# Performance work log

Measured on AMD Instinct MI355X. Metric: run time of the kernel, lower is better.

Reference implementation:

```python
import jax, jax.numpy as jnp
import numpy as np

B, T, IN, H = 131072, 8, 6, 64

def _lstm_layer(x, Wih, Whh, bih, bhh):
    # x: (B, T, in) -> h_seq: (B, T, H). PyTorch gate order: i, f, g, o.
    xg = jnp.einsum('bti,gi->btg', x, Wih) + bih + bhh  # (B, T, 4H)
    Bsz = x.shape[0]
    h0 = jnp.zeros((Bsz, Whh.shape[1]), x.dtype)
    c0 = jnp.zeros_like(h0)
    def step(carry, xg_t):
        h, c = carry
        g = xg_t + h @ Whh.T  # (B, 4H)
        i, f, gg, o = jnp.split(g, 4, axis=-1)
        i = jax.nn.sigmoid(i); f = jax.nn.sigmoid(f)
        gg = jnp.tanh(gg); o = jax.nn.sigmoid(o)
        c = f * c + i * gg
        h = o * jnp.tanh(c)
        return (h, c), h
    _, h_seq = jax.lax.scan(step, (h0, c0), jnp.swapaxes(xg, 0, 1))  # (T, B, H)
    return jnp.swapaxes(h_seq, 0, 1)

def setup_inputs() -> dict:
    key = jax.random.key(0)
    ks = jax.random.split(key, 11)
    s_in = 1.0 / np.sqrt(H)
    u = lambda k, shape: jax.random.uniform(k, shape, jnp.float32, -s_in, s_in)
    return {
        'x': jax.random.normal(ks[0], (B, T, IN), jnp.float32),
        'Wih0': u(ks[1], (4 * H, IN)), 'Whh0': u(ks[2], (4 * H, H)),
        'bih0': u(ks[3], (4 * H,)),   'bhh0': u(ks[4], (4 * H,)),
        'Wih1': u(ks[5], (4 * H, H)), 'Whh1': u(ks[6], (4 * H, H)),
        'bih1': u(ks[7], (4 * H,)),   'bhh1': u(ks[8], (4 * H,)),
        'Wfc': u(ks[9], (1, H)),      'bfc': u(ks[10], (1,)),
    }

def reference(x, Wih0, Whh0, bih0, bhh0, Wih1, Whh1, bih1, bhh1, Wfc, bfc):
    h1 = _lstm_layer(x, Wih0, Whh0, bih0, bhh0)   # (B, T, H)
    # inter-layer dropout & output dropout are identity in eval mode
    h2 = _lstm_layer(h1, Wih1, Whh1, bih1, bhh1)  # (B, T, H)
    last = h2[:, -1, :]                            # (B, H)
    out = last @ Wfc.T + bfc                       # (B, 1)
    return out[:, 0]
```

## Files before the change

### kernel.cpp

```cpp
#include <hip/hip_runtime.h>

#define BLOCK 256
#define TT 8
#define INP 6
#define HDIM 64
#define LDH 72

typedef _Float16 f16;
typedef __attribute__((ext_vector_type(8))) _Float16 f16x8;
typedef __attribute__((ext_vector_type(16))) float f32x16;

#define WIH0_OFF 0
#define WHH0_OFF 4096
#define WIH1_OFF 20480
#define WHH1_OFF 36864
#define H0_OFF   53248
#define H1_OFF   (53248 + 128*LDH)
#define NF16     (53248 + 2*128*LDH)
#define NF32     640

__device__ __forceinline__ float sigm(float x){
    return __builtin_amdgcn_rcpf(1.0f + __builtin_exp2f(-1.442695040888963f*x));
}
__device__ __forceinline__ float ftanh(float x){
    return 1.0f - 2.0f*__builtin_amdgcn_rcpf(1.0f + __builtin_exp2f(2.885390081777927f*x));
}

__global__ void __launch_bounds__(BLOCK, 1)
lstm_mfma(const float* __restrict__ x,
          const float* __restrict__ Wih0, const float* __restrict__ Whh0,
          const float* __restrict__ bih0, const float* __restrict__ bhh0,
          const float* __restrict__ Wih1, const float* __restrict__ Whh1,
          const float* __restrict__ bih1, const float* __restrict__ bhh1,
          const float* __restrict__ Wfc,  const float* __restrict__ bfc,
          float* __restrict__ out)
{
    extern __shared__ char smem[];
    float* fbias = (float*)smem;
    float* fwfc  = fbias + 512;
    f16*   fh    = (f16*)(smem + NF32*4);

    const int tid = threadIdx.x;

    for (int i = tid; i < 3*16384; i += BLOCK){
        int m  = i >> 14;
        int j  = i & 16383;
        int e  = j & 7;
        int l2 = (j >> 3) & 63;
        int fg = j >> 9;
        int n  = (fg >> 2)*32 + (l2 & 31);
        int k  = (fg & 3)*16 + (l2 >> 5)*8 + e;
        const float* W = (m==0)? Whh0 : (m==1)? Wih1 : Whh1;
        int off = (m==0)? WHH0_OFF : (m==1)? WIH1_OFF : WHH1_OFF;
        fh[off + fg*512 + (j & 511)] = (f16)W[n*HDIM + k];
    }
    for (int i = tid; i < 4096; i += BLOCK){
        int e = i & 7, l2 = (i >> 3) & 63, nt = i >> 9;
        int n = nt*32 + (l2 & 31);
        int k = (l2 >> 5)*8 + e;
        fh[WIH0_OFF + nt*512 + (i & 511)] = (k < INP)? (f16)Wih0[n*INP + k] : (f16)0.0f;
    }
    for (int i = tid; i < 256; i += BLOCK){
        fbias[i]       = bih0[i] + bhh0[i];
        fbias[256 + i] = bih1[i] + bhh1[i];
    }
    if (tid < 64) fwfc[tid] = Wfc[tid];
    if (tid == 0) fwfc[64] = bfc[0];
    __syncthreads();

    const int l     = tid & 63;
    const int w     = tid >> 6;
    const int rlo   = l & 31;
    const int khalf = l >> 5;
    const int row0  = blockIdx.x*128 + w*32;

    f16* h0p = fh + H0_OFF + (w*32)*LDH;
    f16* h1p = fh + H1_OFF + (w*32)*LDH;

    float c0[32], c1[32];
#pragma unroll
    for (int i=0;i<32;i++){ c0[i]=0.f; c1[i]=0.f; }

    const float* xrow = x + (size_t)(row0 + rlo)*TT*INP;

#pragma unroll 1
    for (int t=0;t<TT;t++){
        f16x8 xf;
#pragma unroll
        for (int i2=0;i2<8;i2++) xf[i2] = (f16)0.f;
        if (khalf == 0){
            const float* xp = xrow + t*INP;
            xf[0]=(f16)xp[0]; xf[1]=(f16)xp[1]; xf[2]=(f16)xp[2];
            xf[3]=(f16)xp[3]; xf[4]=(f16)xp[4]; xf[5]=(f16)xp[5];
        }

        f32x16 acc[8];
#pragma unroll
        for (int nt=0;nt<8;nt++){
            float bv = fbias[nt*32 + rlo];
#pragma unroll
            for (int r=0;r<16;r++) acc[nt][r] = bv;
        }
#pragma unroll
        for (int nt=0;nt<8;nt++){
            f16x8 bf = *(const f16x8*)(fh + WIH0_OFF + nt*512 + l*8);
            acc[nt] = __builtin_amdgcn_mfma_f32_32x32x16_f16(xf, bf, acc[nt], 0,0,0);
        }
        if (t > 0){
#pragma unroll
            for (int kt=0;kt<4;kt++){
                f16x8 hf = *(const f16x8*)(h0p + rlo*LDH + kt*16 + khalf*8);
#pragma unroll
                for (int nt=0;nt<8;nt++){
                    f16x8 bf = *(const f16x8*)(fh + WHH0_OFF + (nt*4+kt)*512 + l*8);
                    acc[nt] = __builtin_amdgcn_mfma_f32_32x32x16_f16(hf, bf, acc[nt], 0,0,0);
                }
            }
        }
#pragma unroll
        for (int s=0;s<2;s++){
#pragma unroll
            for (int r=0;r<16;r++){
                float ig = sigm (acc[0+s][r]);
                float fg = sigm (acc[2+s][r]);
                float gg = ftanh(acc[4+s][r]);
                float og = sigm (acc[6+s][r]);
                float c  = fg*c0[s*16+r] + ig*gg;
                c0[s*16+r] = c;
                float hv = og*ftanh(c);
                h0p[((r&3) + 8*(r>>2) + 4*khalf)*LDH + rlo + 32*s] = (f16)hv;
            }
        }
        __syncthreads();

#pragma unroll
        for (int nt=0;nt<8;nt++){
            float bv = fbias[256 + nt*32 + rlo];
#pragma unroll
            for (int r=0;r<16;r++) acc[nt][r] = bv;
        }
#pragma unroll
        for (int kt=0;kt<4;kt++){
            f16x8 hf = *(const f16x8*)(h0p + rlo*LDH + kt*16 + khalf*8);
#pragma unroll
            for (int nt=0;nt<8;nt++){
                f16x8 bf = *(const f16x8*)(fh + WIH1_OFF + (nt*4+kt)*512 + l*8);
                acc[nt] = __builtin_amdgcn_mfma_f32_32x32x16_f16(hf, bf, acc[nt], 0,0,0);
            }
        }
        if (t > 0){
#pragma unroll
            for (int kt=0;kt<4;kt++){
                f16x8 hf = *(const f16x8*)(h1p + rlo*LDH + kt*16 + khalf*8);
#pragma unroll
                for (int nt=0;nt<8;nt++){
                    f16x8 bf = *(const f16x8*)(fh + WHH1_OFF + (nt*4+kt)*512 + l*8);
                    acc[nt] = __builtin_amdgcn_mfma_f32_32x32x16_f16(hf, bf, acc[nt], 0,0,0);
                }
            }
        }
#pragma unroll
        for (int s=0;s<2;s++){
#pragma unroll
            for (int r=0;r<16;r++){
                float ig = sigm (acc[0+s][r]);
                float fg = sigm (acc[2+s][r]);
                float gg = ftanh(acc[4+s][r]);
                float og = sigm (acc[6+s][r]);
                float c  = fg*c1[s*16+r] + ig*gg;
                c1[s*16+r] = c;
                float hv = og*ftanh(c);
                h1p[((r&3) + 8*(r>>2) + 4*khalf)*LDH + rlo + 32*s] = (f16)hv;
            }
        }
        __syncthreads();
    }

    if (tid < 128){
        const f16* hp = fh + H1_OFF + tid*LDH;
        float sacc = fwfc[64];
#pragma unroll
        for (int u=0;u<HDIM;u++) sacc += fwfc[u]*(float)hp[u];
        out[(size_t)blockIdx.x*128 + tid] = sacc;
    }
}

extern "C" void kernel_launch(void* const* d_in, const int* in_sizes, int n_in,
                              void* d_out, int out_size, void* d_ws, size_t ws_size,
                              hipStream_t stream) {
    const float* x    = (const float*)d_in[0];
    const float* Wih0 = (const float*)d_in[1];
    const float* Whh0 = (const float*)d_in[2];
    const float* bih0 = (const float*)d_in[3];
    const float* bhh0 = (const float*)d_in[4];
    const float* Wih1 = (const float*)d_in[5];
    const float* Whh1 = (const float*)d_in[6];
    const float* bih1 = (const float*)d_in[7];
    const float* bhh1 = (const float*)d_in[8];
    const float* Wfc  = (const float*)d_in[9];
    const float* bfc  = (const float*)d_in[10];
    float* out = (float*)d_out;

    const int B = in_sizes[0] / (TT*INP);
    const size_t shmem = (size_t)NF32*4 + (size_t)NF16*2;
    hipFuncSetAttribute(reinterpret_cast<const void*>(lstm_mfma),
                        hipFuncAttributeMaxDynamicSharedMemorySize, (int)shmem);
    lstm_mfma<<<dim3(B/128), dim3(BLOCK), shmem, stream>>>(
        x, Wih0, Whh0, bih0, bhh0, Wih1, Whh1, bih1, bhh1, Wfc, bfc, out);
}
```

Measured before the change: 482.5 us.

## Swap MFMA operands so hidden state stays in registers, drop LDS h buffers

The MFMA operand roles are swapped: weights become the A operand and the hidden state the B operand, so each gate output lands in the layout the next step needs. The hidden state is then repacked in registers with a cross-half shuffle instead of going through LDS, which removes both __syncthreads per step. Biases are folded into the matmuls (an extra ones column for layer 0, a small bias-fragment MFMA for layer 1), and the final FC is accumulated during the last step. The block grows to 512 threads with launch bounds allowing 2 blocks per CU, which may increase register pressure or cause spills.

```diff
diff --git a/kernel.cpp b/kernel.cpp
--- a/kernel.cpp
+++ b/kernel.cpp
@@ -1,23 +1,22 @@
 #include <hip/hip_runtime.h>
 
-#define BLOCK 256
+#define BLOCK 512
 #define TT 8
 #define INP 6
 #define HDIM 64
-#define LDH 72
 
 typedef _Float16 f16;
 typedef __attribute__((ext_vector_type(8))) _Float16 f16x8;
 typedef __attribute__((ext_vector_type(16))) float f32x16;
-
-#define WIH0_OFF 0
-#define WHH0_OFF 4096
-#define WIH1_OFF 20480
-#define WHH1_OFF 36864
-#define H0_OFF   53248
-#define H1_OFF   (53248 + 128*LDH)
-#define NF16     (53248 + 2*128*LDH)
-#define NF32     640
+typedef __attribute__((ext_vector_type(4))) int int4v;
+
+#define WHH0_F  0
+#define WIH1_F  16384
+#define WHH1_F  32768
+#define WIH0_F  49152
+#define WIH1B_F 53248
+#define LDS_F16 57344
+#define LDS_BYTES (LDS_F16*2 + 66*4)
 
 __device__ __forceinline__ float sigm(float x){
     return __builtin_amdgcn_rcpf(1.0f + __builtin_exp2f(-1.442695040888963f*x));
@@ -25,9 +24,14 @@
 __device__ __forceinline__ float ftanh(float x){
     return 1.0f - 2.0f*__builtin_amdgcn_rcpf(1.0f + __builtin_exp2f(2.885390081777927f*x));
 }
-
-__global__ void __launch_bounds__(BLOCK, 1)
-lstm_mfma(const float* __restrict__ x,
+__device__ __forceinline__ unsigned pk2(float a, float b){
+    union { f16 h[2]; unsigned u; } uu;
+    uu.h[0] = (f16)a; uu.h[1] = (f16)b;
+    return uu.u;
+}
+
+__global__ void __launch_bounds__(BLOCK, 2)
+lstm_swap(const float* __restrict__ x,
           const float* __restrict__ Wih0, const float* __restrict__ Whh0,
           const float* __restrict__ bih0, const float* __restrict__ bhh0,
           const float* __restrict__ Wih1, const float* __restrict__ Whh1,
@@ -36,153 +40,153 @@
           float* __restrict__ out)
 {
     extern __shared__ char smem[];
-    float* fbias = (float*)smem;
-    float* fwfc  = fbias + 512;
-    f16*   fh    = (f16*)(smem + NF32*4);
+    f16*   fh = (f16*)smem;
+    float* fw = (float*)(smem + LDS_F16*2);
 
     const int tid = threadIdx.x;
 
     for (int i = tid; i < 3*16384; i += BLOCK){
-        int m  = i >> 14;
-        int j  = i & 16383;
-        int e  = j & 7;
-        int l2 = (j >> 3) & 63;
-        int fg = j >> 9;
-        int n  = (fg >> 2)*32 + (l2 & 31);
-        int k  = (fg & 3)*16 + (l2 >> 5)*8 + e;
+        int m = i >> 14, j = i & 16383, fg = j >> 9, jj = j & 511;
+        int e = jj & 7, l2 = jj >> 3;
+        int nt = fg >> 2, kt = fg & 3;
+        int n = nt*32 + (l2 & 31), k = kt*16 + (l2 >> 5)*8 + e;
         const float* W = (m==0)? Whh0 : (m==1)? Wih1 : Whh1;
-        int off = (m==0)? WHH0_OFF : (m==1)? WIH1_OFF : WHH1_OFF;
-        fh[off + fg*512 + (j & 511)] = (f16)W[n*HDIM + k];
+        int base = (m==0)? WHH0_F : (m==1)? WIH1_F : WHH1_F;
+        fh[base + fg*512 + jj] = (f16)W[n*HDIM + k];
     }
     for (int i = tid; i < 4096; i += BLOCK){
-        int e = i & 7, l2 = (i >> 3) & 63, nt = i >> 9;
-        int n = nt*32 + (l2 & 31);
-        int k = (l2 >> 5)*8 + e;
-        fh[WIH0_OFF + nt*512 + (i & 511)] = (k < INP)? (f16)Wih0[n*INP + k] : (f16)0.0f;
-    }
-    for (int i = tid; i < 256; i += BLOCK){
-        fbias[i]       = bih0[i] + bhh0[i];
-        fbias[256 + i] = bih1[i] + bhh1[i];
-    }
-    if (tid < 64) fwfc[tid] = Wfc[tid];
-    if (tid == 0) fwfc[64] = bfc[0];
+        int fg = i >> 9, jj = i & 511, e = jj & 7, l2 = jj >> 3;
+        int n = fg*32 + (l2 & 31), k = (l2 >> 5)*8 + e;
+        float v = (k < INP) ? Wih0[n*INP + k] : (k == INP ? bih0[n] + bhh0[n] : 0.f);
+        fh[WIH0_F + fg*512 + jj] = (f16)v;
+    }
+    for (int i = tid; i < 4096; i += BLOCK){
+        int fg = i >> 9, jj = i & 511, e = jj & 7, l2 = jj >> 3;
+        int n = fg*32 + (l2 & 31);
+        float v = ((l2 >> 5) == 0 && e == 0) ? bih1[n] + bhh1[n] : 0.f;
+        fh[WIH1B_F + fg*512 + jj] = (f16)v;
+    }
+    if (tid < 64) fw[tid] = Wfc[tid];
+    if (tid == 0) fw[64] = bfc[0];
     __syncthreads();
 
     const int l     = tid & 63;
     const int w     = tid >> 6;
-    const int rlo   = l & 31;
+    const int cb    = l & 31;
     const int khalf = l >> 5;
-    const int row0  = blockIdx.x*128 + w*32;
-
-    f16* h0p = fh + H0_OFF + (w*32)*LDH;
-    f16* h1p = fh + H1_OFF + (w*32)*LDH;
-
+    const int brow  = blockIdx.x*(BLOCK/64)*32 + w*32 + cb;
+
+    const float* xrow = x + (size_t)brow*(TT*INP);
+
+#define AFRAG(BASE, IDX) (*(const f16x8*)(fh + (BASE) + (IDX)*512 + l*8))
+
+    int4v h0f[4], h1f[4];
+#pragma unroll
+    for (int k2=0;k2<4;k2++){ h0f[k2] = (int4v)0; h1f[k2] = (int4v)0; }
     float c0[32], c1[32];
 #pragma unroll
     for (int i=0;i<32;i++){ c0[i]=0.f; c1[i]=0.f; }
 
-    const float* xrow = x + (size_t)(row0 + rlo)*TT*INP;
+    f16x8 biasb;
+#pragma unroll
+    for (int i=0;i<8;i++) biasb[i] = (f16)0.f;
+    if (khalf == 0) biasb[0] = (f16)1.0f;
+
+    float fc = 0.f;
+
+#define GATES(CARR, HF, DO_FC)                                                     \
+    _Pragma("unroll")                                                              \
+    for (int bb=0; bb<4; bb++){                                                    \
+        const int nt2 = bb>>1, rbase = 8*(bb&1);                                   \
+        float hvv[8];                                                              \
+        _Pragma("unroll")                                                          \
+        for (int rr=0; rr<8; rr++){                                                \
+            const int r = rbase + rr;                                              \
+            float iv = sigm (acc[nt2+0][r]);                                       \
+            float fv = sigm (acc[nt2+2][r]);                                       \
+            float gv = ftanh(acc[nt2+4][r]);                                       \
+            float ov = sigm (acc[nt2+6][r]);                                       \
+            float cc = fv*CARR[nt2*16+r] + iv*gv;                                  \
+            CARR[nt2*16+r] = cc;                                                   \
+            float hv = ov*ftanh(cc);                                               \
+            hvv[rr] = hv;                                                          \
+            if (DO_FC) fc += fw[nt2*32 + (r&3) + 8*(r>>2) + 4*khalf]*hv;           \
+        }                                                                          \
+        unsigned X0 = pk2(hvv[0],hvv[1]), X1 = pk2(hvv[2],hvv[3]);                 \
+        unsigned Y0 = pk2(hvv[4],hvv[5]), Y1 = pk2(hvv[6],hvv[7]);                 \
+        unsigned s0 = khalf ? X0 : Y0;                                             \
+        unsigned s1 = khalf ? X1 : Y1;                                             \
+        unsigned r0 = __shfl_xor(s0, 32);                                          \
+        unsigned r1 = __shfl_xor(s1, 32);                                          \
+        int F0 = khalf ? (int)r0 : (int)X0;                                        \
+        int F1 = khalf ? (int)r1 : (int)X1;                                        \
+        int F2 = khalf ? (int)Y0 : (int)r0;                                        \
+        int F3 = khalf ? (int)Y1 : (int)r1;                                        \
+        HF[bb] = (int4v){F0, F1, F2, F3};                                          \
+    }
 
 #pragma unroll 1
-    for (int t=0;t<TT;t++){
+    for (int t=0; t<TT; t++){
+        float2 xv0 = *(const float2*)(xrow + t*INP);
+        float2 xv1 = *(const float2*)(xrow + t*INP + 2);
+        float2 xv2 = *(const float2*)(xrow + t*INP + 4);
+
+        f32x16 acc[8];
+#pragma unroll
+        for (int nt=0; nt<8; nt++)
+#pragma unroll
+            for (int r=0; r<16; r++) acc[nt][r] = 0.f;
+
+#pragma unroll
+        for (int kt=0; kt<4; kt++){
+            f16x8 b = __builtin_bit_cast(f16x8, h0f[kt]);
+#pragma unroll
+            for (int nt=0; nt<8; nt++)
+                acc[nt] = __builtin_amdgcn_mfma_f32_32x32x16_f16(AFRAG(WHH0_F, nt*4+kt), b, acc[nt], 0,0,0);
+        }
         f16x8 xf;
 #pragma unroll
-        for (int i2=0;i2<8;i2++) xf[i2] = (f16)0.f;
+        for (int i=0;i<8;i++) xf[i] = (f16)0.f;
         if (khalf == 0){
-            const float* xp = xrow + t*INP;
-            xf[0]=(f16)xp[0]; xf[1]=(f16)xp[1]; xf[2]=(f16)xp[2];
-            xf[3]=(f16)xp[3]; xf[4]=(f16)xp[4]; xf[5]=(f16)xp[5];
-        }
-
-        f32x16 acc[8];
-#pragma unroll
-        for (int nt=0;nt<8;nt++){
-            float bv = fbias[nt*32 + rlo];
-#pragma unroll
-            for (int r=0;r<16;r++) acc[nt][r] = bv;
-        }
-#pragma unroll
-        for (int nt=0;nt<8;nt++){
-            f16x8 bf = *(const f16x8*)(fh + WIH0_OFF + nt*512 + l*8);
-            acc[nt] = __builtin_amdgcn_mfma_f32_32x32x16_f16(xf, bf, acc[nt], 0,0,0);
-        }
-        if (t > 0){
-#pragma unroll
-            for (int kt=0;kt<4;kt++){
-                f16x8 hf = *(const f16x8*)(h0p + rlo*LDH + kt*16 + khalf*8);
-#pragma unroll
-                for (int nt=0;nt<8;nt++){
-                    f16x8 bf = *(const f16x8*)(fh + WHH0_OFF + (nt*4+kt)*512 + l*8);
-                    acc[nt] = __builtin_amdgcn_mfma_f32_32x32x16_f16(hf, bf, acc[nt], 0,0,0);
-                }
-            }
-        }
-#pragma unroll
-        for (int s=0;s<2;s++){
-#pragma unroll
-            for (int r=0;r<16;r++){
-                float ig = sigm (acc[0+s][r]);
-                float fg = sigm (acc[2+s][r]);
-                float gg = ftanh(acc[4+s][r]);
-                float og = sigm (acc[6+s][r]);
-                float c  = fg*c0[s*16+r] + ig*gg;
-                c0[s*16+r] = c;
-                float hv = og*ftanh(c);
-                h0p[((r&3) + 8*(r>>2) + 4*khalf)*LDH + rlo + 32*s] = (f16)hv;
-            }
-        }
-        __syncthreads();
-
-#pragma unroll
-        for (int nt=0;nt<8;nt++){
-            float bv = fbias[256 + nt*32 + rlo];
-#pragma unroll
-            for (int r=0;r<16;r++) acc[nt][r] = bv;
-        }
-#pragma unroll
-        for (int kt=0;kt<4;kt++){
-            f16x8 hf = *(const f16x8*)(h0p + rlo*LDH + kt*16 + khalf*8);
-#pragma unroll
-            for (int nt=0;nt<8;nt++){
-                f16x8 bf = *(const f16x8*)(fh + WIH1_OFF + (nt*4+kt)*512 + l*8);
-                acc[nt] = __builtin_amdgcn_mfma_f32_32x32x16_f16(hf, bf, acc[nt], 0,0,0);
-            }
-        }
-        if (t > 0){
-#pragma unroll
-            for (int kt=0;kt<4;kt++){
-                f16x8 hf = *(const f16x8*)(h1p + rlo*LDH + kt*16 + khalf*8);
-#pragma unroll
-                for (int nt=0;nt<8;nt++){
-                    f16x8 bf = *(const f16x8*)(fh + WHH1_OFF + (nt*4+kt)*512 + l*8);
-                    acc[nt] = __builtin_amdgcn_mfma_f32_32x32x16_f16(hf, bf, acc[nt], 0,0,0);
-                }
-            }
-        }
-#pragma unroll
-        for (int s=0;s<2;s++){
-#pragma unroll
-            for (int r=0;r<16;r++){
-                float ig = sigm (acc[0+s][r]);
-                float fg = sigm (acc[2+s][r]);
-                float gg = ftanh(acc[4+s][r]);
-                float og = sigm (acc[6+s][r]);
-                float c  = fg*c1[s*16+r] + ig*gg;
-                c1[s*16+r] = c;
-                float hv = og*ftanh(c);
-                h1p[((r&3) + 8*(r>>2) + 4*khalf)*LDH + rlo + 32*s] = (f16)hv;
-            }
-        }
-        __syncthreads();
-    }
-
-    if (tid < 128){
-        const f16* hp = fh + H1_OFF + tid*LDH;
-        float sacc = fwfc[64];
-#pragma unroll
-        for (int u=0;u<HDIM;u++) sacc += fwfc[u]*(float)hp[u];
-        out[(size_t)blockIdx.x*128 + tid] = sacc;
-    }
+            xf[0]=(f16)xv0.x; xf[1]=(f16)xv0.y; xf[2]=(f16)xv1.x;
+            xf[3]=(f16)xv1.y; xf[4]=(f16)xv2.x; xf[5]=(f16)xv2.y;
+            xf[6]=(f16)1.0f;
+        }
+#pragma unroll
+        for (int nt=0; nt<8; nt++)
+            acc[nt] = __builtin_amdgcn_mfma_f32_32x32x16_f16(AFRAG(WIH0_F, nt), xf, acc[nt], 0,0,0);
+
+        GATES(c0, h0f, false)
+
+#pragma unroll
+        for (int nt=0; nt<8; nt++)
+#pragma unroll
+            for (int r=0; r<16; r++) acc[nt][r] = 0.f;
+#pragma unroll
+        for (int kt=0; kt<4; kt++){
+            f16x8 b = __builtin_bit_cast(f16x8, h0f[kt]);
+#pragma unroll
+            for (int nt=0; nt<8; nt++)
+                acc[nt] = __builtin_amdgcn_mfma_f32_32x32x16_f16(AFRAG(WIH1_F, nt*4+kt), b, acc[nt], 0,0,0);
+        }
+#pragma unroll
+        for (int nt=0; nt<8; nt++)
+            acc[nt] = __builtin_amdgcn_mfma_f32_32x32x16_f16(AFRAG(WIH1B_F, nt), biasb, acc[nt], 0,0,0);
+#pragma unroll
+        for (int kt=0; kt<4; kt++){
+            f16x8 b = __builtin_bit_cast(f16x8, h1f[kt]);
+#pragma unroll
+            for (int nt=0; nt<8; nt++)
+                acc[nt] = __builtin_amdgcn_mfma_f32_32x32x16_f16(AFRAG(WHH1_F, nt*4+kt), b, acc[nt], 0,0,0);
+        }
+
+        GATES(c1, h1f, (t == TT-1))
+    }
+
+    float so = __shfl_xor(fc, 32);
+    float tot = fc + so + fw[64];
+    if (l < 32)
+        out[(size_t)blockIdx.x*(BLOCK/64)*32 + w*32 + l] = tot;
 }
 
 extern "C" void kernel_launch(void* const* d_in, const int* in_sizes, int n_in,
@@ -202,9 +206,10 @@
     float* out = (float*)d_out;
 
     const int B = in_sizes[0] / (TT*INP);
-    const size_t shmem = (size_t)NF32*4 + (size_t)NF16*2;
-    hipFuncSetAttribute(reinterpret_cast<const void*>(lstm_mfma),
+    const int rows_per_block = (BLOCK/64)*32;
+    const size_t shmem = LDS_BYTES;
+    hipFuncSetAttribute(reinterpret_cast<const void*>(lstm_swap),
                         hipFuncAttributeMaxDynamicSharedMemorySize, (int)shmem);
-    lstm_mfma<<<dim3(B/128), dim3(BLOCK), shmem, stream>>>(
+    lstm_swap<<<dim3(B/rows_per_block), dim3(BLOCK), shmem, stream>>>(
         x, Wih0, Whh0, bih0, bhh0, Wih1, Whh1, bih1, bhh1, Wfc, bfc, out);
 }
```

Measured after the change: 1.277 ms. 165% more time.
